# Performance work log

Hardware: AMD Instinct MI355X
Metric: run time of the kernel (lower is better)

## Reference

```python
import jax, jax.numpy as jnp
import numpy as np

SELECTED_NUM = 4096
BN_EPS = 1e-5


def _conv1d(x, w, pad):
    # x: [B, C_in, L], w: [C_out, C_in, K]
    return jax.lax.conv_general_dilated(
        x, w, window_strides=(1,), padding=[(pad, pad)],
        dimension_numbers=('NCH', 'OIH', 'NCH'))


def _bn(x, g, b, m, v):
    # eval-mode BatchNorm1d over channel dim of [B, C, L]
    inv = g / jnp.sqrt(v + BN_EPS)
    return x * inv[None, :, None] + (b - m * inv)[None, :, None]


def setup_inputs() -> dict:
    key = jax.random.key(0)
    ks = jax.random.split(key, 16)
    B, N, CODE, NCLS = 4, 262144, 7, 3
    inp = {
        'box_preds': jax.random.normal(ks[0], (B, N, CODE), jnp.float32),
        'cls_preds': jax.random.normal(ks[1], (B, N, NCLS), jnp.float32),
        # conv_share: Conv1d(10,32,3) + BN(32) + ReLU + Conv1d(32,64,3) + BN(64) + ReLU
        'conv1_w': jax.random.normal(ks[2], (32, 10, 3), jnp.float32) * 0.1,
        'bn1_g': jax.random.uniform(ks[3], (32,), jnp.float32, 0.5, 1.5),
        'bn1_b': jax.random.normal(ks[4], (32,), jnp.float32) * 0.1,
        'bn1_m': jax.random.normal(ks[5], (32,), jnp.float32) * 0.1,
        'bn1_v': jax.random.uniform(ks[6], (32,), jnp.float32, 0.5, 1.5),
        'conv2_w': jax.random.normal(ks[7], (64, 32, 3), jnp.float32) * 0.1,
        'bn2_g': jax.random.uniform(ks[8], (64,), jnp.float32, 0.5, 1.5),
        'bn2_b': jax.random.normal(ks[9], (64,), jnp.float32) * 0.1,
        'bn2_m': jax.random.normal(ks[10], (64,), jnp.float32) * 0.1,
        'bn2_v': jax.random.uniform(ks[11], (64,), jnp.float32, 0.5, 1.5),
        # heads: Conv1d(64,5,1,bias=True), Conv1d(64,1,1,bias=True)
        'bin_w': jax.random.normal(ks[12], (5, 64, 1), jnp.float32) * 0.1,
        'bin_b': jnp.full((5,), -float(np.log((1 - 0.01) / 0.01)), jnp.float32),
        'res_w': jax.random.normal(ks[13], (1, 64, 1), jnp.float32) * 0.001,
        'res_b': jnp.zeros((1,), jnp.float32),
    }
    return inp


def reference(box_preds, cls_preds, conv1_w, bn1_g, bn1_b, bn1_m, bn1_v,
              conv2_w, bn2_g, bn2_b, bn2_m, bn2_v, bin_w, bin_b, res_w, res_b):
    # ---- proposal_layer: per-batch sigmoid(max-cls-score) topk + gather ----
    score = jax.nn.sigmoid(jnp.max(cls_preds, axis=-1))          # [B, N]
    _, sel = jax.lax.top_k(score, SELECTED_NUM)                  # [B, K]
    box_sel = jnp.take_along_axis(box_preds, sel[:, :, None], axis=1)  # [B, K, 7]
    cls_sel = jnp.take_along_axis(cls_preds, sel[:, :, None], axis=1)  # [B, K, 3]

    # ---- conv_share + heads over channel-first layout [B, 10, K] ----
    x = jnp.concatenate([box_sel, cls_sel], axis=-1).transpose(0, 2, 1)  # [B, 10, K]
    x = jax.nn.relu(_bn(_conv1d(x, conv1_w, 1), bn1_g, bn1_b, bn1_m, bn1_v))
    x = jax.nn.relu(_bn(_conv1d(x, conv2_w, 1), bn2_g, bn2_b, bn2_m, bn2_v))  # [B, 64, K]

    iou_bin = _conv1d(x, bin_w, 0) + bin_b[None, :, None]        # [B, 5, K]
    iou_res = _conv1d(x, res_w, 0) + res_b[None, :, None]        # [B, 1, K]

    iou_preds_bin = iou_bin.transpose(0, 2, 1)                   # [B, K, 5]
    iou_preds_residual = iou_res.transpose(0, 2, 1)              # [B, K, 1]
    return iou_preds_bin, iou_preds_residual, box_sel, cls_sel
```

## Files before the change

### kernel.cpp

```cpp
#include <hip/hip_runtime.h>
#include <stdint.h>

#define NPTS 262144
#define NB 4
#define KSEL 4096
#define CAP 8192
#define SLICE_LEN 1024
#define CBLK 128
#define HBLK 64

#define OFF_BITS  0ULL
#define OFF_H8P   (4ULL*NPTS*NB)
#define OFF_H12   (OFF_H8P + 4ULL*256*HBLK*NB)
#define OFF_CTRL  (OFF_H12 + 4ULL*4096*NB)
#define OFF_GRANK (OFF_CTRL + 1024ULL)
#define OFF_CAND  (OFF_GRANK + 4ULL*CAP*NB)
#define WS_NEEDED (OFF_CAND + 8ULL*CAP*NB)

#define OBIN 0
#define ORES (NB*KSEL*5)
#define OBOX (ORES + NB*KSEL)
#define OCLS (OBOX + NB*KSEL*7)


__device__ __forceinline__ uint32_t key_of(float mx) {
    uint32_t b = __float_as_uint(mx);
    uint32_t mask = ((int32_t)b >> 31) | 0x80000000u;
    return b ^ mask;
}

__device__ __forceinline__ void suffix_scan_256(volatile uint32_t* part, int tid) {
    #pragma unroll
    for (int off = 1; off < 256; off <<= 1) {
        uint32_t v = part[tid] + ((tid + off < 256) ? part[tid + off] : 0u);
        __syncthreads();
        part[tid] = v;
        __syncthreads();
    }
}

__global__ __launch_bounds__(256) void k_score_hist(
    const float* __restrict__ cls, uint32_t* __restrict__ bits, uint32_t* __restrict__ h8p,
    uint32_t* __restrict__ h12, uint32_t* __restrict__ grank, uint32_t* __restrict__ ctrl)
{
    __shared__ uint32_t lh[8][256];
    for (int i = threadIdx.x; i < 2048; i += 256) ((uint32_t*)lh)[i] = 0;
    __syncthreads();
    int b = blockIdx.y, bx = blockIdx.x;
    int sub = threadIdx.x >> 5;
    for (int it = 0; it < 4; ++it) {
        int chunk = bx * 1024 + it * 256 + threadIdx.x;
        const float4* p = (const float4*)(cls + ((size_t)b * NPTS + (size_t)chunk * 4) * 3);
        float4 v0 = p[0], v1 = p[1], v2 = p[2];
        uint4 o;
        o.x = key_of(fmaxf(fmaxf(v0.x, v0.y), v0.z));
        o.y = key_of(fmaxf(fmaxf(v0.w, v1.x), v1.y));
        o.z = key_of(fmaxf(fmaxf(v1.z, v1.w), v2.x));
        o.w = key_of(fmaxf(fmaxf(v2.y, v2.z), v2.w));
        ((uint4*)(bits + (size_t)b * NPTS))[chunk] = o;
        atomicAdd(&lh[sub][o.x >> 24], 1u);
        atomicAdd(&lh[sub][o.y >> 24], 1u);
        atomicAdd(&lh[sub][o.z >> 24], 1u);
        atomicAdd(&lh[sub][o.w >> 24], 1u);
    }
    if (bx == 1) {
        uint4* z = (uint4*)(h12 + (size_t)b * 4096);
        #pragma unroll
        for (int i = 0; i < 4; ++i) z[threadIdx.x + i * 256] = make_uint4(0u, 0u, 0u, 0u);
    } else if (bx == 2) {
        uint4* zg = (uint4*)(grank + (size_t)b * CAP);
        #pragma unroll
        for (int i = 0; i < 8; ++i) zg[threadIdx.x + i * 256] = make_uint4(0u, 0u, 0u, 0u);
    } else if (bx == 3 && threadIdx.x == 0) {
        ctrl[b * 16 + 3] = 0u;
    }
    __syncthreads();
    uint32_t c = 0;
    #pragma unroll
    for (int s = 0; s < 8; ++s) c += lh[s][threadIdx.x];
    h8p[((size_t)b * HBLK + bx) * 256 + threadIdx.x] = c;
}

__global__ __launch_bounds__(256) void k_hist12(
    const uint32_t* __restrict__ bits, const uint32_t* __restrict__ h8p,
    uint32_t* __restrict__ ctrl, uint32_t* __restrict__ h12)
{
    __shared__ uint32_t lh[4096];
    __shared__ uint32_t part[257];
    __shared__ uint32_t P8s;
    int b = blockIdx.y, bx = blockIdx.x;
    int tid = threadIdx.x;
    for (int i = tid; i < 4096; i += 256) lh[i] = 0;
    uint32_t sum = 0;
    const uint32_t* hp = h8p + (size_t)b * HBLK * 256 + tid;
    #pragma unroll 8
    for (int blk = 0; blk < HBLK; ++blk) sum += hp[blk * 256];
    part[tid] = sum;
    if (tid == 0) part[256] = 0u;
    __syncthreads();
    suffix_scan_256(part, tid);
    {
        uint32_t si = part[tid], sn = part[tid + 1];
        if (si >= (uint32_t)KSEL && sn < (uint32_t)KSEL) {
            P8s = (uint32_t)tid;
            if (bx == 0) { ctrl[b * 16 + 0] = (uint32_t)tid; ctrl[b * 16 + 1] = sn; }
        }
    }
    __syncthreads();
    const uint32_t P8 = P8s;
    for (int it = 0; it < 4; ++it) {
        int chunk = bx * 1024 + it * 256 + tid;
        uint4 v = ((const uint4*)(bits + (size_t)b * NPTS))[chunk];
        if ((v.x >> 24) == P8) atomicAdd(&lh[(v.x >> 12) & 0xFFFu], 1u);
        if ((v.y >> 24) == P8) atomicAdd(&lh[(v.y >> 12) & 0xFFFu], 1u);
        if ((v.z >> 24) == P8) atomicAdd(&lh[(v.z >> 12) & 0xFFFu], 1u);
        if ((v.w >> 24) == P8) atomicAdd(&lh[(v.w >> 12) & 0xFFFu], 1u);
    }
    __syncthreads();
    for (int i = tid; i < 4096; i += 256) {
        uint32_t c = lh[i];
        if (c) atomicAdd(&h12[(size_t)b * 4096 + i], c);
    }
}

__global__ __launch_bounds__(256) void k_compact(
    const uint32_t* __restrict__ bits, const uint32_t* __restrict__ h12,
    uint32_t* __restrict__ ctrl, uint64_t* __restrict__ cand)
{
    __shared__ uint32_t bins[4096];
    __shared__ uint32_t part[257];
    __shared__ uint32_t segS, Ts;
    __shared__ uint32_t wbase[4];
    int b = blockIdx.y, bx = blockIdx.x;
    int tid = threadIdx.x;
    const uint4* src = (const uint4*)(h12 + (size_t)b * 4096);
    for (int i = tid; i < 1024; i += 256) ((uint4*)bins)[i] = src[i];
    __syncthreads();
    {
        uint32_t s = 0;
        int base2 = tid * 16;
        #pragma unroll
        for (int j = 0; j < 16; ++j) s += bins[base2 + j];
        part[tid] = s;
        if (tid == 0) part[256] = 0u;
    }
    __syncthreads();
    const uint32_t K = (uint32_t)KSEL - ctrl[b * 16 + 1];
    suffix_scan_256(part, tid);
    {
        uint32_t si = part[tid], sn = part[tid + 1];
        if (si >= K && sn < K) segS = (uint32_t)tid;
    }
    __syncthreads();
    if (tid < 16) {
        uint32_t seg = segS;
        uint32_t above = part[seg + 1];
        uint32_t cnt = above;
        for (int j = 15; j >= tid; --j) cnt += bins[seg * 16 + j];
        uint32_t cntn = cnt - bins[seg * 16 + tid];
        if (cnt >= K && cntn < K)
            Ts = (ctrl[b * 16 + 0] << 12) | (seg * 16 + (uint32_t)tid);
    }
    __syncthreads();
    const uint32_t T = Ts;
    const int lane = tid & 63, wave = tid >> 6;
    const uint64_t lmask = (1ull << lane) - 1ull;

    int chunk0 = bx * 512 + tid;
    const uint4* sb = (const uint4*)(bits + (size_t)b * NPTS);
    uint4 v0 = sb[chunk0];
    uint4 v1 = sb[chunk0 + 256];
    uint32_t ks[8] = {v0.x, v0.y, v0.z, v0.w, v1.x, v1.y, v1.z, v1.w};
    bool sel[8];
    #pragma unroll
    for (int i = 0; i < 8; ++i) sel[i] = (ks[i] >> 12) >= T;

    uint32_t wsum = 0;
    #pragma unroll
    for (int i = 0; i < 8; ++i) wsum += (uint32_t)__popcll(__ballot(sel[i]));
    if (lane == 0) wbase[wave] = wsum;
    __syncthreads();
    if (tid == 0) {
        uint32_t c0 = wbase[0], c1 = wbase[1], c2 = wbase[2], c3 = wbase[3];
        uint32_t tot = c0 + c1 + c2 + c3;
        uint32_t base = tot ? atomicAdd(&ctrl[b * 16 + 3], tot) : 0u;
        wbase[0] = base;
        wbase[1] = base + c0;
        wbase[2] = base + c0 + c1;
        wbase[3] = base + c0 + c1 + c2;
    }
    __syncthreads();
    uint32_t off = wbase[wave];
    #pragma unroll
    for (int i = 0; i < 8; ++i) {
        uint64_t m = __ballot(sel[i]);
        if (sel[i]) {
            uint32_t pos = off + (uint32_t)__popcll(m & lmask);
            uint32_t n = (uint32_t)(chunk0 + (i < 4 ? 0 : 256)) * 4 + (uint32_t)(i & 3);
            if (pos < CAP)
                cand[(size_t)b * CAP + pos] = ((uint64_t)(~ks[i]) << 32) | (uint64_t)n;
        }
        off += (uint32_t)__popcll(m);
    }
}

__global__ __launch_bounds__(256) void k_rank1(
    const uint64_t* __restrict__ cand, const uint32_t* __restrict__ ctrl,
    uint32_t* __restrict__ grank)
{
    __shared__ uint64_t keys[SLICE_LEN];
    int b = blockIdx.z;
    uint32_t C = ctrl[b * 16 + 3];
    if (C > CAP) C = CAP;
    uint32_t ig0 = blockIdx.x * 256;
    uint32_t sk0 = blockIdx.y * SLICE_LEN;
    if (ig0 >= C || sk0 >= C) return;
    uint32_t nk = C - sk0; if (nk > SLICE_LEN) nk = SLICE_LEN;
    const uint64_t* cb = cand + (size_t)b * CAP;
    for (uint32_t i = threadIdx.x; i < nk; i += 256) keys[i] = cb[sk0 + i];
    __syncthreads();
    uint32_t item = ig0 + threadIdx.x;
    if (item >= C) return;
    uint64_t me = cb[item];
    uint32_t r = 0;
    #pragma unroll 16
    for (uint32_t i = 0; i < nk; ++i) r += (keys[i] < me) ? 1u : 0u;
    atomicAdd(&grank[b * CAP + item], r);
}

__global__ __launch_bounds__(256) void k_rank2(
    const uint64_t* __restrict__ cand, const uint32_t* __restrict__ ctrl,
    const uint32_t* __restrict__ grank,
    const float* __restrict__ box, const float* __restrict__ cls, float* __restrict__ out)
{
    int b = blockIdx.y;
    uint32_t C = ctrl[b * 16 + 3];
    if (C > CAP) C = CAP;
    uint32_t item = blockIdx.x * 256 + threadIdx.x;
    if (blockIdx.x * 256 >= C) return;
    if (item >= C) return;
    uint64_t me = cand[(size_t)b * CAP + item];
    uint32_t rank = grank[b * CAP + item];
    if (rank < KSEL) {
        uint32_t n = (uint32_t)me;
        const float* bp = box + ((size_t)b * NPTS + n) * 7;
        float* ob = out + OBOX + ((size_t)b * KSEL + rank) * 7;
        #pragma unroll
        for (int c = 0; c < 7; ++c) ob[c] = bp[c];
        const float* cp = cls + ((size_t)b * NPTS + n) * 3;
        float* oc = out + OCLS + ((size_t)b * KSEL + rank) * 3;
        #pragma unroll
        for (int c = 0; c < 3; ++c) oc[c] = cp[c];
    }
}

__global__ __launch_bounds__(256) void k_conv(
    const float* __restrict__ c1w, const float* __restrict__ g1v, const float* __restrict__ b1v,
    const float* __restrict__ m1v, const float* __restrict__ v1v,
    const float* __restrict__ c2w, const float* __restrict__ g2v, const float* __restrict__ b2v,
    const float* __restrict__ m2v, const float* __restrict__ v2v,
    const float* __restrict__ binw, const float* __restrict__ binb,
    const float* __restrict__ resw, const float* __restrict__ resb,
    float* __restrict__ out)
{
    __shared__ __align__(16) float w1s[960];
    __shared__ __align__(16) float b1s[32];
    __shared__ __align__(16) float w2s[6144];
    __shared__ __align__(16) float b2s[64];
    __shared__ __align__(16) float hws[6][64];
    __shared__ __align__(16) float xin[10][80];
    __shared__ __align__(16) float x1s[32][68];
    __shared__ __align__(16) float x2t[64][68];

    int tid = threadIdx.x;
    int b = blockIdx.y;
    int tile0 = blockIdx.x * 64;
    const float* boxsel = out + OBOX + (size_t)b * KSEL * 7;
    const float* clssel = out + OCLS + (size_t)b * KSEL * 3;

    for (int t = tid; t < 960; t += 256) {
        int c = t / 30, r = t - c * 30, i = r / 3, tap = r - i * 3;
        float inv = g1v[c] * rsqrtf(v1v[c] + 1e-5f);
        w1s[(i * 3 + tap) * 32 + c] = c1w[t] * inv;
    }
    if (tid < 32) {
        float inv = g1v[tid] * rsqrtf(v1v[tid] + 1e-5f);
        b1s[tid] = b1v[tid] - m1v[tid] * inv;
    }
    for (int t = tid; t < 6144; t += 256) {
        int o = t / 96, r = t - o * 96, i = r / 3, tap = r - i * 3;
        float inv = g2v[o] * rsqrtf(v2v[o] + 1e-5f);
        w2s[(i * 3 + tap) * 64 + o] = c2w[t] * inv;
    }
    if (tid >= 64 && tid < 128) {
        int o = tid - 64;
        float inv = g2v[o] * rsqrtf(v2v[o] + 1e-5f);
        b2s[o] = b2v[o] - m2v[o] * inv;
    }
    for (int t = tid; t < 384; t += 256)
        ((float*)hws)[t] = (t < 320) ? binw[t] : resw[t - 320];

    for (int u = tid; u < 680; u += 256) {
        int c = u / 68, k2 = u - c * 68;
        int g = tile0 + k2 - 2;
        float val = 0.f;
        if (g >= 0 && g < KSEL) val = (c < 7) ? boxsel[g * 7 + c] : clssel[g * 3 + (c - 7)];
        xin[c][k2] = val;
    }
    __syncthreads();

    {
        int c = tid & 31, kg = tid >> 5;
        int k0 = kg * 9;
        int nk = 66 - k0; if (nk > 9) nk = 9;
        float a[9];
        #pragma unroll
        for (int kk = 0; kk < 9; ++kk) a[kk] = b1s[c];
        #pragma unroll 2
        for (int i = 0; i < 10; ++i) {
            float xv[11];
            #pragma unroll
            for (int j = 0; j < 11; ++j) xv[j] = xin[i][k0 + j];
            #pragma unroll
            for (int tap = 0; tap < 3; ++tap) {
                float w = w1s[(i * 3 + tap) * 32 + c];
                #pragma unroll
                for (int kk = 0; kk < 9; ++kk) a[kk] = fmaf(w, xv[kk + tap], a[kk]);
            }
        }
        for (int kk = 0; kk < nk; ++kk) {
            int k = k0 + kk, gp = tile0 + k - 1;
            x1s[c][k] = (gp >= 0 && gp < KSEL) ? fmaxf(a[kk], 0.f) : 0.f;
        }
    }
    __syncthreads();

    {
        int o = tid & 63, pg = tid >> 6;
        int p0 = pg * 16;
        float acc[16];
        float bz = b2s[o];
        #pragma unroll
        for (int kk = 0; kk < 16; ++kk) acc[kk] = bz;
        #pragma unroll 4
        for (int i = 0; i < 32; ++i) {
            float4 xq[5];
            const float4* xr = (const float4*)&x1s[i][p0];
            #pragma unroll
            for (int q = 0; q < 5; ++q) xq[q] = xr[q];
            const float* xf = (const float*)xq;
            float w0 = w2s[(i * 3 + 0) * 64 + o];
            float w1 = w2s[(i * 3 + 1) * 64 + o];
            float w2 = w2s[(i * 3 + 2) * 64 + o];
            #pragma unroll
            for (int kk = 0; kk < 16; ++kk) {
                float t0 = fmaf(w0, xf[kk], acc[kk]);
                t0 = fmaf(w1, xf[kk + 1], t0);
                acc[kk] = fmaf(w2, xf[kk + 2], t0);
            }
        }
        #pragma unroll
        for (int kk = 0; kk < 16; ++kk)
            x2t[p0 + kk][o] = fmaxf(acc[kk], 0.f);
    }
    __syncthreads();

    {
        int p = tid & 63, g = tid >> 6;
        const float4* xr = (const float4*)&x2t[p][0];
        const float4* hw4 = (const float4*)hws;
        size_t gpos = (size_t)b * KSEL + (size_t)(tile0 + p);
        if (g < 2) {
            int j0 = g * 2, j1 = j0 + 1;
            float s0 = 0.f, s1 = 0.f;
            #pragma unroll
            for (int q = 0; q < 16; ++q) {
                float4 xv = xr[q];
                float4 wa = hw4[j0 * 16 + q];
                float4 wb = hw4[j1 * 16 + q];
                s0 = fmaf(xv.x, wa.x, s0); s0 = fmaf(xv.y, wa.y, s0);
                s0 = fmaf(xv.z, wa.z, s0); s0 = fmaf(xv.w, wa.w, s0);
                s1 = fmaf(xv.x, wb.x, s1); s1 = fmaf(xv.y, wb.y, s1);
                s1 = fmaf(xv.z, wb.z, s1); s1 = fmaf(xv.w, wb.w, s1);
            }
            out[OBIN + gpos * 5 + j0] = s0 + binb[j0];
            out[OBIN + gpos * 5 + j1] = s1 + binb[j1];
        } else {
            int j = (g == 2) ? 4 : 5;
            float s = 0.f;
            #pragma unroll
            for (int q = 0; q < 16; ++q) {
                float4 xv = xr[q];
                float4 wa = hw4[j * 16 + q];
                s = fmaf(xv.x, wa.x, s); s = fmaf(xv.y, wa.y, s);
                s = fmaf(xv.z, wa.z, s); s = fmaf(xv.w, wa.w, s);
            }
            if (g == 2) out[OBIN + gpos * 5 + 4] = s + binb[4];
            else        out[ORES + gpos]         = s + resb[0];
        }
    }
}

extern "C" void kernel_launch(void* const* d_in, const int* in_sizes, int n_in,
                              void* d_out, int out_size, void* d_ws, size_t ws_size,
                              hipStream_t stream)
{
    const float* box  = (const float*)d_in[0];
    const float* cls  = (const float*)d_in[1];
    const float* c1w  = (const float*)d_in[2];
    const float* g1   = (const float*)d_in[3];
    const float* b1   = (const float*)d_in[4];
    const float* m1   = (const float*)d_in[5];
    const float* v1   = (const float*)d_in[6];
    const float* c2w  = (const float*)d_in[7];
    const float* g2   = (const float*)d_in[8];
    const float* b2   = (const float*)d_in[9];
    const float* m2   = (const float*)d_in[10];
    const float* v2   = (const float*)d_in[11];
    const float* binw = (const float*)d_in[12];
    const float* binb = (const float*)d_in[13];
    const float* resw = (const float*)d_in[14];
    const float* resb = (const float*)d_in[15];
    float* out = (float*)d_out;
    char* ws = (char*)d_ws;
    if (ws_size < WS_NEEDED) return;

    uint32_t* bits  = (uint32_t*)(ws + OFF_BITS);
    uint32_t* h8p   = (uint32_t*)(ws + OFF_H8P);
    uint32_t* h12   = (uint32_t*)(ws + OFF_H12);
    uint32_t* ctrl  = (uint32_t*)(ws + OFF_CTRL);
    uint32_t* grank = (uint32_t*)(ws + OFF_GRANK);
    uint64_t* cand  = (uint64_t*)(ws + OFF_CAND);

    k_score_hist<<<dim3(HBLK, NB), 256, 0, stream>>>(cls, bits, h8p, h12, grank, ctrl);
    k_hist12<<<dim3(HBLK, NB), 256, 0, stream>>>(bits, h8p, ctrl, h12);
    k_compact<<<dim3(CBLK, NB), 256, 0, stream>>>(bits, h12, ctrl, cand);
    k_rank1<<<dim3(CAP / 256, 8, NB), 256, 0, stream>>>(cand, ctrl, grank);
    k_rank2<<<dim3(CAP / 256, NB), 256, 0, stream>>>(cand, ctrl, grank, box, cls, out);
    k_conv<<<dim3(64, NB), 256, 0, stream>>>(c1w, g1, b1, m1, v1, c2w, g2, b2, m2, v2,
                                             binw, binb, resw, resb, out);
}
```

Baseline: 68.89 us.

## Replace two-pass 8+12-bit radix histogram with single-pass 13-bit histogram

The top-k threshold search used to take two passes: an 8-bit histogram, then a second 12-bit histogram over the selected bucket, with a re-read of the keys in between. It now builds one 8192-bin histogram on the top 13 key bits while computing scores, and merges it globally with atomics. The compact kernel finds the threshold directly from that histogram, which removes one pass over the 4 MB of keys and one kernel launch. In exchange it adds a small zeroing kernel, uses more shared memory and global atomics per block, and gives a coarser threshold, so more candidates may pass compaction and could approach the CAP limit.

```diff
diff --git a/kernel.cpp b/kernel.cpp
--- a/kernel.cpp
+++ b/kernel.cpp
@@ -8,11 +8,11 @@
 #define SLICE_LEN 1024
 #define CBLK 128
 #define HBLK 64
+#define NBIN 8192
 
 #define OFF_BITS  0ULL
-#define OFF_H8P   (4ULL*NPTS*NB)
-#define OFF_H12   (OFF_H8P + 4ULL*256*HBLK*NB)
-#define OFF_CTRL  (OFF_H12 + 4ULL*4096*NB)
+#define OFF_H13   (4ULL*NPTS*NB)
+#define OFF_CTRL  (OFF_H13 + 4ULL*NBIN*NB)
 #define OFF_GRANK (OFF_CTRL + 1024ULL)
 #define OFF_CAND  (OFF_GRANK + 4ULL*CAP*NB)
 #define WS_NEEDED (OFF_CAND + 8ULL*CAP*NB)
@@ -39,15 +39,19 @@
     }
 }
 
-__global__ __launch_bounds__(256) void k_score_hist(
-    const float* __restrict__ cls, uint32_t* __restrict__ bits, uint32_t* __restrict__ h8p,
-    uint32_t* __restrict__ h12, uint32_t* __restrict__ grank, uint32_t* __restrict__ ctrl)
-{
-    __shared__ uint32_t lh[8][256];
-    for (int i = threadIdx.x; i < 2048; i += 256) ((uint32_t*)lh)[i] = 0;
+__global__ __launch_bounds__(256) void k_init(uint4* __restrict__ h13v)
+{
+    h13v[blockIdx.x * 256 + threadIdx.x] = make_uint4(0u, 0u, 0u, 0u);
+}
+
+__global__ __launch_bounds__(256) void k_score(
+    const float* __restrict__ cls, uint32_t* __restrict__ bits, uint32_t* __restrict__ h13,
+    uint32_t* __restrict__ grank, uint32_t* __restrict__ ctrl)
+{
+    __shared__ uint32_t lh[NBIN];
+    for (int i = threadIdx.x; i < NBIN; i += 256) lh[i] = 0;
     __syncthreads();
     int b = blockIdx.y, bx = blockIdx.x;
-    int sub = threadIdx.x >> 5;
     for (int it = 0; it < 4; ++it) {
         int chunk = bx * 1024 + it * 256 + threadIdx.x;
         const float4* p = (const float4*)(cls + ((size_t)b * NPTS + (size_t)chunk * 4) * 3);
@@ -58,108 +62,62 @@
         o.z = key_of(fmaxf(fmaxf(v1.z, v1.w), v2.x));
         o.w = key_of(fmaxf(fmaxf(v2.y, v2.z), v2.w));
         ((uint4*)(bits + (size_t)b * NPTS))[chunk] = o;
-        atomicAdd(&lh[sub][o.x >> 24], 1u);
-        atomicAdd(&lh[sub][o.y >> 24], 1u);
-        atomicAdd(&lh[sub][o.z >> 24], 1u);
-        atomicAdd(&lh[sub][o.w >> 24], 1u);
+        atomicAdd(&lh[o.x >> 19], 1u);
+        atomicAdd(&lh[o.y >> 19], 1u);
+        atomicAdd(&lh[o.z >> 19], 1u);
+        atomicAdd(&lh[o.w >> 19], 1u);
     }
     if (bx == 1) {
-        uint4* z = (uint4*)(h12 + (size_t)b * 4096);
-        #pragma unroll
-        for (int i = 0; i < 4; ++i) z[threadIdx.x + i * 256] = make_uint4(0u, 0u, 0u, 0u);
-    } else if (bx == 2) {
         uint4* zg = (uint4*)(grank + (size_t)b * CAP);
         #pragma unroll
         for (int i = 0; i < 8; ++i) zg[threadIdx.x + i * 256] = make_uint4(0u, 0u, 0u, 0u);
-    } else if (bx == 3 && threadIdx.x == 0) {
+    } else if (bx == 2 && threadIdx.x == 0) {
         ctrl[b * 16 + 3] = 0u;
     }
     __syncthreads();
-    uint32_t c = 0;
-    #pragma unroll
-    for (int s = 0; s < 8; ++s) c += lh[s][threadIdx.x];
-    h8p[((size_t)b * HBLK + bx) * 256 + threadIdx.x] = c;
-}
-
-__global__ __launch_bounds__(256) void k_hist12(
-    const uint32_t* __restrict__ bits, const uint32_t* __restrict__ h8p,
-    uint32_t* __restrict__ ctrl, uint32_t* __restrict__ h12)
-{
-    __shared__ uint32_t lh[4096];
-    __shared__ uint32_t part[257];
-    __shared__ uint32_t P8s;
-    int b = blockIdx.y, bx = blockIdx.x;
-    int tid = threadIdx.x;
-    for (int i = tid; i < 4096; i += 256) lh[i] = 0;
-    uint32_t sum = 0;
-    const uint32_t* hp = h8p + (size_t)b * HBLK * 256 + tid;
-    #pragma unroll 8
-    for (int blk = 0; blk < HBLK; ++blk) sum += hp[blk * 256];
-    part[tid] = sum;
-    if (tid == 0) part[256] = 0u;
-    __syncthreads();
-    suffix_scan_256(part, tid);
-    {
-        uint32_t si = part[tid], sn = part[tid + 1];
-        if (si >= (uint32_t)KSEL && sn < (uint32_t)KSEL) {
-            P8s = (uint32_t)tid;
-            if (bx == 0) { ctrl[b * 16 + 0] = (uint32_t)tid; ctrl[b * 16 + 1] = sn; }
-        }
-    }
-    __syncthreads();
-    const uint32_t P8 = P8s;
-    for (int it = 0; it < 4; ++it) {
-        int chunk = bx * 1024 + it * 256 + tid;
-        uint4 v = ((const uint4*)(bits + (size_t)b * NPTS))[chunk];
-        if ((v.x >> 24) == P8) atomicAdd(&lh[(v.x >> 12) & 0xFFFu], 1u);
-        if ((v.y >> 24) == P8) atomicAdd(&lh[(v.y >> 12) & 0xFFFu], 1u);
-        if ((v.z >> 24) == P8) atomicAdd(&lh[(v.z >> 12) & 0xFFFu], 1u);
-        if ((v.w >> 24) == P8) atomicAdd(&lh[(v.w >> 12) & 0xFFFu], 1u);
-    }
-    __syncthreads();
-    for (int i = tid; i < 4096; i += 256) {
+    uint32_t* h13b = h13 + (size_t)b * NBIN;
+    for (int i = threadIdx.x; i < NBIN; i += 256) {
         uint32_t c = lh[i];
-        if (c) atomicAdd(&h12[(size_t)b * 4096 + i], c);
+        if (c) atomicAdd(&h13b[i], c);
     }
 }
 
 __global__ __launch_bounds__(256) void k_compact(
-    const uint32_t* __restrict__ bits, const uint32_t* __restrict__ h12,
+    const uint32_t* __restrict__ bits, const uint32_t* __restrict__ h13,
     uint32_t* __restrict__ ctrl, uint64_t* __restrict__ cand)
 {
-    __shared__ uint32_t bins[4096];
+    __shared__ uint32_t bins[NBIN];
     __shared__ uint32_t part[257];
     __shared__ uint32_t segS, Ts;
     __shared__ uint32_t wbase[4];
     int b = blockIdx.y, bx = blockIdx.x;
     int tid = threadIdx.x;
-    const uint4* src = (const uint4*)(h12 + (size_t)b * 4096);
-    for (int i = tid; i < 1024; i += 256) ((uint4*)bins)[i] = src[i];
+    const uint4* src = (const uint4*)(h13 + (size_t)b * NBIN);
+    for (int i = tid; i < NBIN / 4; i += 256) ((uint4*)bins)[i] = src[i];
     __syncthreads();
     {
         uint32_t s = 0;
-        int base2 = tid * 16;
-        #pragma unroll
-        for (int j = 0; j < 16; ++j) s += bins[base2 + j];
+        int base2 = tid * 32;
+        #pragma unroll
+        for (int j = 0; j < 32; ++j) s += bins[base2 + j];
         part[tid] = s;
         if (tid == 0) part[256] = 0u;
     }
     __syncthreads();
-    const uint32_t K = (uint32_t)KSEL - ctrl[b * 16 + 1];
     suffix_scan_256(part, tid);
     {
         uint32_t si = part[tid], sn = part[tid + 1];
-        if (si >= K && sn < K) segS = (uint32_t)tid;
-    }
-    __syncthreads();
-    if (tid < 16) {
+        if (si >= (uint32_t)KSEL && sn < (uint32_t)KSEL) segS = (uint32_t)tid;
+    }
+    __syncthreads();
+    if (tid < 32) {
         uint32_t seg = segS;
         uint32_t above = part[seg + 1];
         uint32_t cnt = above;
-        for (int j = 15; j >= tid; --j) cnt += bins[seg * 16 + j];
-        uint32_t cntn = cnt - bins[seg * 16 + tid];
-        if (cnt >= K && cntn < K)
-            Ts = (ctrl[b * 16 + 0] << 12) | (seg * 16 + (uint32_t)tid);
+        for (int j = 31; j >= tid; --j) cnt += bins[seg * 32 + j];
+        uint32_t cntn = cnt - bins[seg * 32 + tid];
+        if (cnt >= (uint32_t)KSEL && cntn < (uint32_t)KSEL)
+            Ts = seg * 32 + (uint32_t)tid;
     }
     __syncthreads();
     const uint32_t T = Ts;
@@ -173,7 +131,7 @@
     uint32_t ks[8] = {v0.x, v0.y, v0.z, v0.w, v1.x, v1.y, v1.z, v1.w};
     bool sel[8];
     #pragma unroll
-    for (int i = 0; i < 8; ++i) sel[i] = (ks[i] >> 12) >= T;
+    for (int i = 0; i < 8; ++i) sel[i] = (ks[i] >> 19) >= T;
 
     uint32_t wsum = 0;
     #pragma unroll
@@ -426,15 +384,14 @@
     if (ws_size < WS_NEEDED) return;
 
     uint32_t* bits  = (uint32_t*)(ws + OFF_BITS);
-    uint32_t* h8p   = (uint32_t*)(ws + OFF_H8P);
-    uint32_t* h12   = (uint32_t*)(ws + OFF_H12);
+    uint32_t* h13   = (uint32_t*)(ws + OFF_H13);
     uint32_t* ctrl  = (uint32_t*)(ws + OFF_CTRL);
     uint32_t* grank = (uint32_t*)(ws + OFF_GRANK);
     uint64_t* cand  = (uint64_t*)(ws + OFF_CAND);
 
-    k_score_hist<<<dim3(HBLK, NB), 256, 0, stream>>>(cls, bits, h8p, h12, grank, ctrl);
-    k_hist12<<<dim3(HBLK, NB), 256, 0, stream>>>(bits, h8p, ctrl, h12);
-    k_compact<<<dim3(CBLK, NB), 256, 0, stream>>>(bits, h12, ctrl, cand);
+    k_init<<<(NBIN * NB) / 1024, 256, 0, stream>>>((uint4*)h13);
+    k_score<<<dim3(HBLK, NB), 256, 0, stream>>>(cls, bits, h13, grank, ctrl);
+    k_compact<<<dim3(CBLK, NB), 256, 0, stream>>>(bits, h13, ctrl, cand);
     k_rank1<<<dim3(CAP / 256, 8, NB), 256, 0, stream>>>(cand, ctrl, grank);
     k_rank2<<<dim3(CAP / 256, NB), 256, 0, stream>>>(cand, ctrl, grank, box, cls, out);
     k_conv<<<dim3(64, NB), 256, 0, stream>>>(c1w, g1, b1, m1, v1, c2w, g2, b2, m2, v2,
```

Result: no change. 68.48 us, median of 2 (-0.6%).
